# Performance work log

Measured on AMD Instinct MI355X. Metric: run time of the kernel, lower is better.

The kernel has to match this reference:

```python
import jax, jax.numpy as jnp
import numpy as np

B, T, H, NSPK = 8, 1024, 1024, 2
LN_EPS = 1e-5


def setup_inputs() -> dict:
    key = jax.random.key(0)
    ks = jax.random.split(key, 12)
    s = 1.0 / np.sqrt(H)
    return {
        "x": jax.random.normal(ks[0], (B, T, H), jnp.float32),
        "qmask": jax.random.uniform(ks[1], (B, T, NSPK), jnp.float32),
        "dia_len": jax.random.randint(ks[2], (B,), T // 2, T + 1),
        "wp": 8,
        "wf": 8,
        "W_msg": jax.random.normal(ks[3], (H, H), jnp.float32) * s,
        "b_msg": jax.random.normal(ks[4], (H,), jnp.float32) * s,
        "W_self": jax.random.normal(ks[5], (H, H), jnp.float32) * s,
        "b_self": jax.random.normal(ks[6], (H,), jnp.float32) * s,
        "W_out": jax.random.normal(ks[7], (H, H), jnp.float32) * s,
        "b_out": jax.random.normal(ks[8], (H,), jnp.float32) * s,
        "gamma": jnp.ones((H,), jnp.float32),
        "beta": jnp.zeros((H,), jnp.float32),
    }


def reference(x, qmask, dia_len, wp, wf, W_msg, b_msg, W_self, b_self, W_out, b_out, gamma, beta):
    Bb, Tt, Hh = x.shape
    spk = jnp.argmax(qmask, axis=-1)                     # [B,T]
    pos = jnp.arange(Tt)
    offs = jnp.arange(-wp, wf + 1)                       # [W]
    idx = pos[:, None] + offs[None, :]                   # [T,W] window indices
    vlen = dia_len[:, None, None]                        # [B,1,1]
    valid = (idx[None] >= 0) & (idx[None] <= vlen - 1)   # [B,T,W]
    idxc = jnp.clip(idx, 0, Tt - 1)
    nb = jnp.take(x, idxc, axis=1)                       # [B,T,W,H]
    nb_spk = jnp.take(spk, idxc, axis=1)                 # [B,T,W]
    same = (nb_spk == spk[:, :, None]).astype(x.dtype)
    w = jnp.where(valid, 0.5 + 0.5 * same, 0.0)          # speaker weights, masked
    cnt = jnp.maximum(valid.sum(-1).astype(x.dtype), 1.0)  # window sizes [B,T]
    msg = jnp.einsum('btw,btwh->bth', w, nb) / cnt[..., None]
    h = x @ W_self + b_self + msg @ W_msg + b_msg        # per-node fusion
    node_valid = (pos[None, :] < dia_len[:, None])[..., None]
    out = jnp.where(node_valid, h, x)                    # nodes past dia_len keep x
    y = jax.nn.relu(out) @ W_out + b_out                 # dropout = identity (eval)
    z = x + y
    mean = z.mean(-1, keepdims=True)
    var = z.var(-1, keepdims=True)
    return gamma * (z - mean) / jnp.sqrt(var + LN_EPS) + beta
```

## Files before the change

### kernel.cpp

```cpp
#include <hip/hip_runtime.h>


typedef unsigned short u16;
typedef float floatx4 __attribute__((ext_vector_type(4)));
typedef short shortx8 __attribute__((ext_vector_type(8)));

#define T_ 1024
#define H_ 1024

__device__ __forceinline__ float bf2f(u16 v) {
    return __uint_as_float(((unsigned)v) << 16);
}
__device__ __forceinline__ u16 f2bf(float f) {
    unsigned u = __float_as_uint(f);
    return (u16)((u + 0x7fffu + ((u >> 16) & 1u)) >> 16);
}
__device__ __forceinline__ void async16(const void* g, void* l) {
    __builtin_amdgcn_global_load_lds(
        (__attribute__((address_space(1))) void*)g,
        (__attribute__((address_space(3))) void*)l, 16, 0, 0);
}
__device__ __forceinline__ void barrier_mem() {
    asm volatile("" ::: "memory");
    __builtin_amdgcn_s_barrier();
    asm volatile("" ::: "memory");
}

__global__ __launch_bounds__(256)
void transpose_pack(const float* __restrict__ Wself, const float* __restrict__ Wmsg,
                    const float* __restrict__ Wout,
                    u16* __restrict__ wt_cat, u16* __restrict__ wt_out)
{
    __shared__ float s[32][33];
    const int wid = blockIdx.z;
    const float* src = (wid == 0) ? Wself : ((wid == 1) ? Wmsg : Wout);
    const int n0 = blockIdx.x * 32, k0 = blockIdx.y * 32;
    const int tx = threadIdx.x & 31, ty = threadIdx.x >> 5;
#pragma unroll
    for (int i = 0; i < 4; ++i) {
        int k = k0 + ty + 8 * i;
        s[ty + 8 * i][tx] = src[(size_t)k * H_ + n0 + tx];
    }
    __syncthreads();
#pragma unroll
    for (int i = 0; i < 4; ++i) {
        int n = n0 + ty + 8 * i;
        u16 v = f2bf(s[tx][ty + 8 * i]);
        if (wid < 2) wt_cat[(size_t)n * 2048 + wid * 1024 + k0 + tx] = v;
        else         wt_out[(size_t)n * 1024 + k0 + tx] = v;
    }
}

__global__ __launch_bounds__(256)
void msg_pack(const float* __restrict__ x, const float* __restrict__ qmask,
              const int* __restrict__ dia_len, u16* __restrict__ xcat)
{
    __shared__ u16 sx[32][1024];
    const int tid = threadIdx.x;
    const int b = blockIdx.y;
    const int t0 = blockIdx.x * 16;
    const int dlen = dia_len[b];
    const int c4 = tid * 4;
    const float* xb = x + (size_t)b * T_ * H_;

    unsigned spkmask = 0;
#pragma unroll 4
    for (int r = 0; r < 32; ++r) {
        int row = t0 - 8 + r;
        row = row < 0 ? 0 : (row > T_ - 1 ? T_ - 1 : row);
        const float* q = qmask + ((size_t)b * T_ + row) * 2;
        spkmask |= (q[1] > q[0] ? 1u : 0u) << r;
        float4 v = *(const float4*)(xb + (size_t)row * H_ + c4);
        ushort4 u;
        u.x = f2bf(v.x); u.y = f2bf(v.y); u.z = f2bf(v.z); u.w = f2bf(v.w);
        *(ushort4*)&sx[r][c4] = u;
    }
    __syncthreads();

    for (int lt = 0; lt < 16; ++lt) {
        const int t = t0 + lt;
        const unsigned cs = (spkmask >> (lt + 8)) & 1u;
        float a0 = 0.f, a1 = 0.f, a2 = 0.f, a3 = 0.f;
        int cnt = 0;
#pragma unroll
        for (int o = 0; o < 17; ++o) {
            const int idx = t + o - 8;
            if (idx >= 0 && idx < dlen) {
                const float w = (((spkmask >> (lt + o)) & 1u) == cs) ? 1.0f : 0.5f;
                ++cnt;
                ushort4 u = *(const ushort4*)&sx[lt + o][c4];
                a0 += w * bf2f(u.x); a1 += w * bf2f(u.y);
                a2 += w * bf2f(u.z); a3 += w * bf2f(u.w);
            }
        }
        const float inv = 1.0f / (float)(cnt > 0 ? cnt : 1);
        ushort4 m;
        m.x = f2bf(a0 * inv); m.y = f2bf(a1 * inv);
        m.z = f2bf(a2 * inv); m.w = f2bf(a3 * inv);
        const size_t rowg = (size_t)b * T_ + t;
        *(ushort4*)&xcat[rowg * 2048 + 1024 + c4] = m;
        *(ushort4*)&xcat[rowg * 2048 + c4] = *(const ushort4*)&sx[lt + 8][c4];
    }
}

template <int K, int EPI>
__global__ __launch_bounds__(512)
void gemm_bt(const u16* __restrict__ A, const u16* __restrict__ Bt,
             const float* __restrict__ bias1, const float* __restrict__ bias2,
             const float* __restrict__ X, const int* __restrict__ dia_len,
             u16* __restrict__ Rout, float* __restrict__ Zout)
{
    constexpr int NT = K / 64;
    static_assert(NT >= 3, "need >=3 K-tiles for depth-2 prefetch");
    __shared__ u16 sA[3][256 * 64];
    __shared__ u16 sB[3][128 * 64];
    const int tid = threadIdx.x;

    const int bid = blockIdx.x;
    const int li = bid >> 3;
    const int mt = (bid & 7) * 4 + (li >> 3);
    const int nt = li & 7;
    const int bm = mt * 256, bn = nt * 128;

    const int wave = tid >> 6, lane = tid & 63;
    const int wr = wave >> 1, wc = wave & 1;
    const int lrow = lane & 15, lq = lane >> 4;

    const int srow = tid >> 3;
    const int sl   = (tid & 7) ^ (srow & 7);
    const u16* Asrc = A + (size_t)(bm + srow) * K + sl * 8;
    const u16* Bsrc = Bt + (size_t)(bn + srow) * K + sl * 8;

    auto stageA = [&](int t, int buf, int q) {
        async16(Asrc + (size_t)q * 64 * K + t * 64,
                &sA[buf][q * 4096 + tid * 8]);
    };
    auto stageB = [&](int t, int buf, int h) {
        async16(Bsrc + (size_t)h * 64 * K + t * 64,
                &sB[buf][h * 4096 + tid * 8]);
    };

    floatx4 acc[4][4];
#pragma unroll
    for (int i = 0; i < 4; ++i)
#pragma unroll
        for (int j = 0; j < 4; ++j)
            acc[i][j] = (floatx4){0.f, 0.f, 0.f, 0.f};

    const int xk = lrow & 7;
    const int paBase = (wr * 64 + lrow) * 64;
    const int pbBase = (wc * 64 + lrow) * 64;
    const int s0 = ((lq) ^ xk) * 8;
    const int s1 = ((4 + lq) ^ xk) * 8;

    auto tile_body = [&](int t, int cur, int stg, bool do_stage) {
        const u16* curA = &sA[cur][0];
        const u16* curB = &sB[cur][0];
        shortx8 a0[4], b0[4], a1[4], b1[4];
#pragma unroll
        for (int j = 0; j < 4; ++j)
            b0[j] = *(const shortx8*)(curB + pbBase + j * 1024 + s0);
#pragma unroll
        for (int i = 0; i < 4; ++i)
            a0[i] = *(const shortx8*)(curA + paBase + i * 1024 + s0);
        if (do_stage) {
            stageA(t + 2, stg, 0); stageA(t + 2, stg, 1);
            stageA(t + 2, stg, 2); stageA(t + 2, stg, 3);
            stageB(t + 2, stg, 0); stageB(t + 2, stg, 1);
        }
#pragma unroll
        for (int j = 0; j < 4; ++j)
            b1[j] = *(const shortx8*)(curB + pbBase + j * 1024 + s1);
#pragma unroll
        for (int i = 0; i < 4; ++i)
            a1[i] = *(const shortx8*)(curA + paBase + i * 1024 + s1);
        __builtin_amdgcn_s_setprio(1);
#pragma unroll
        for (int i = 0; i < 4; ++i)
#pragma unroll
            for (int j = 0; j < 4; ++j)
                acc[i][j] = __builtin_amdgcn_mfma_f32_16x16x32_bf16(
                    a0[i], b0[j], acc[i][j], 0, 0, 0);
#pragma unroll
        for (int i = 0; i < 4; ++i)
#pragma unroll
            for (int j = 0; j < 4; ++j)
                acc[i][j] = __builtin_amdgcn_mfma_f32_16x16x32_bf16(
                    a1[i], b1[j], acc[i][j], 0, 0, 0);
        __builtin_amdgcn_s_setprio(0);
    };

#pragma unroll
    for (int q = 0; q < 4; ++q) stageA(0, 0, q);
    stageB(0, 0, 0); stageB(0, 0, 1);
#pragma unroll
    for (int q = 0; q < 4; ++q) stageA(1, 1, q);
    stageB(1, 1, 0); stageB(1, 1, 1);
    asm volatile("s_waitcnt vmcnt(6)" ::: "memory");
    barrier_mem();

    int cur = 0, stg = 2;
    for (int t = 0; t < NT - 2; ++t) {
        tile_body(t, cur, stg, true);
        asm volatile("s_waitcnt vmcnt(6)" ::: "memory");
        barrier_mem();
        cur = (cur == 2) ? 0 : cur + 1;
        stg = (stg == 2) ? 0 : stg + 1;
    }
    tile_body(NT - 2, cur, stg, false);
    asm volatile("s_waitcnt vmcnt(0)" ::: "memory");
    barrier_mem();
    cur = (cur == 2) ? 0 : cur + 1;
    tile_body(NT - 1, cur, stg, false);

    const int dl = (EPI == 1) ? dia_len[bm >> 10] : 0;
#pragma unroll
    for (int i = 0; i < 4; ++i) {
        const int row0 = bm + wr * 64 + i * 16 + lq * 4;
#pragma unroll
        for (int j = 0; j < 4; ++j) {
            const int col = bn + wc * 64 + j * 16 + lrow;
#pragma unroll
            for (int r = 0; r < 4; ++r) {
                const int row = row0 + r;
                const float v = acc[i][j][r];
                if (EPI == 1) {
                    const float h = v + bias1[col] + bias2[col];
                    float outv;
                    if ((row & (T_ - 1)) < dl) {
                        outv = h;
                    } else {
                        outv = X[(size_t)row * H_ + col];
                    }
                    Rout[(size_t)row * H_ + col] = f2bf(fmaxf(outv, 0.f));
                } else {
                    const float z = X[(size_t)row * H_ + col] + v + bias1[col];
                    Zout[(size_t)row * H_ + col] = z;
                }
            }
        }
    }
}

__global__ __launch_bounds__(256)
void ln_kernel(const float* __restrict__ Z, const float* __restrict__ gamma,
               const float* __restrict__ beta, float* __restrict__ out)
{
    const int row = blockIdx.x;
    const int tid = threadIdx.x;
    const size_t base = (size_t)row * H_ + tid * 4;
    float4 v = *(const float4*)(Z + base);
    float s = v.x + v.y + v.z + v.w;
    float q = v.x * v.x + v.y * v.y + v.z * v.z + v.w * v.w;
#pragma unroll
    for (int off = 32; off > 0; off >>= 1) {
        s += __shfl_down(s, off);
        q += __shfl_down(q, off);
    }
    __shared__ float ps[4], pq[4];
    const int wave = tid >> 6, lane = tid & 63;
    if (lane == 0) { ps[wave] = s; pq[wave] = q; }
    __syncthreads();
    const float S = ps[0] + ps[1] + ps[2] + ps[3];
    const float Q = pq[0] + pq[1] + pq[2] + pq[3];
    const float mean = S * (1.0f / 1024.0f);
    const float var = Q * (1.0f / 1024.0f) - mean * mean;
    const float inv = rsqrtf(var + 1e-5f);
    float4 g = *(const float4*)(gamma + tid * 4);
    float4 bt = *(const float4*)(beta + tid * 4);
    float4 o;
    o.x = g.x * (v.x - mean) * inv + bt.x;
    o.y = g.y * (v.y - mean) * inv + bt.y;
    o.z = g.z * (v.z - mean) * inv + bt.z;
    o.w = g.w * (v.w - mean) * inv + bt.w;
    *(float4*)(out + base) = o;
}

extern "C" void kernel_launch(void* const* d_in, const int* in_sizes, int n_in,
                              void* d_out, int out_size, void* d_ws, size_t ws_size,
                              hipStream_t stream)
{
    (void)in_sizes; (void)n_in; (void)out_size; (void)ws_size;
    const float* x       = (const float*)d_in[0];
    const float* qmask   = (const float*)d_in[1];
    const int*   dia_len = (const int*)d_in[2];
    const float* W_msg   = (const float*)d_in[5];
    const float* b_msg   = (const float*)d_in[6];
    const float* W_self  = (const float*)d_in[7];
    const float* b_self  = (const float*)d_in[8];
    const float* W_out   = (const float*)d_in[9];
    const float* b_out   = (const float*)d_in[10];
    const float* gamma   = (const float*)d_in[11];
    const float* beta    = (const float*)d_in[12];
    float* out = (float*)d_out;

    char* ws = (char*)d_ws;
    u16*   xcat   = (u16*)ws;
    u16*   rbuf   = (u16*)(ws + (size_t)(32u << 20));
    u16*   wt_cat = (u16*)(ws + (size_t)(48u << 20));
    u16*   wt_out = (u16*)(ws + (size_t)(52u << 20));
    float* zbuf   = (float*)ws;

    transpose_pack<<<dim3(32, 32, 3), 256, 0, stream>>>(W_self, W_msg, W_out, wt_cat, wt_out);
    msg_pack<<<dim3(64, 8), 256, 0, stream>>>(x, qmask, dia_len, xcat);
    gemm_bt<2048, 1><<<dim3(256), 512, 0, stream>>>(xcat, wt_cat, b_self, b_msg,
                                                    x, dia_len, rbuf, nullptr);
    gemm_bt<1024, 2><<<dim3(256), 512, 0, stream>>>(rbuf, wt_out, b_out, nullptr,
                                                    x, nullptr, nullptr, zbuf);
    ln_kernel<<<dim3(8192), 256, 0, stream>>>(zbuf, gamma, beta, out);
}
```

Before: 230.8 us.

## Shrink GEMM tiles to 128x128 with 256 threads and double-buffered LDS

Both GEMMs switch from 256x128 tiles with 512 threads and triple-buffered LDS to 128x128 tiles with 256 threads and double buffering, with 2 blocks per CU and twice as many blocks launched. The K loop now prefetches one tile ahead and drains all loads each iteration. The aim is to cut LDS use and raise occupancy so two blocks can hide each other's latency. The cost is less reuse per tile, more global and L2 traffic, and a shallower prefetch pipeline.

```diff
diff --git a/kernel.cpp b/kernel.cpp
--- a/kernel.cpp
+++ b/kernel.cpp
@@ -104,23 +104,23 @@
 }
 
 template <int K, int EPI>
-__global__ __launch_bounds__(512)
+__global__ __launch_bounds__(256, 2)
 void gemm_bt(const u16* __restrict__ A, const u16* __restrict__ Bt,
              const float* __restrict__ bias1, const float* __restrict__ bias2,
              const float* __restrict__ X, const int* __restrict__ dia_len,
              u16* __restrict__ Rout, float* __restrict__ Zout)
 {
     constexpr int NT = K / 64;
-    static_assert(NT >= 3, "need >=3 K-tiles for depth-2 prefetch");
-    __shared__ u16 sA[3][256 * 64];
-    __shared__ u16 sB[3][128 * 64];
+    static_assert(NT >= 2, "need >=2 K-tiles");
+    __shared__ u16 sA[2][128 * 64];
+    __shared__ u16 sB[2][128 * 64];
     const int tid = threadIdx.x;
 
     const int bid = blockIdx.x;
-    const int li = bid >> 3;
-    const int mt = (bid & 7) * 4 + (li >> 3);
+    const int xcd = bid & 7, li = bid >> 3;
+    const int mt = xcd * 8 + (li >> 3);
     const int nt = li & 7;
-    const int bm = mt * 256, bn = nt * 128;
+    const int bm = mt * 128, bn = nt * 128;
 
     const int wave = tid >> 6, lane = tid & 63;
     const int wr = wave >> 1, wc = wave & 1;
@@ -131,13 +131,14 @@
     const u16* Asrc = A + (size_t)(bm + srow) * K + sl * 8;
     const u16* Bsrc = Bt + (size_t)(bn + srow) * K + sl * 8;
 
-    auto stageA = [&](int t, int buf, int q) {
-        async16(Asrc + (size_t)q * 64 * K + t * 64,
-                &sA[buf][q * 4096 + tid * 8]);
-    };
-    auto stageB = [&](int t, int buf, int h) {
-        async16(Bsrc + (size_t)h * 64 * K + t * 64,
-                &sB[buf][h * 4096 + tid * 8]);
+    auto stage = [&](int t, int buf) {
+        const int k0 = t * 64;
+#pragma unroll
+        for (int q = 0; q < 4; ++q)
+            async16(Asrc + (size_t)q * 32 * K + k0, &sA[buf][q * 2048 + tid * 8]);
+#pragma unroll
+        for (int q = 0; q < 4; ++q)
+            async16(Bsrc + (size_t)q * 32 * K + k0, &sB[buf][q * 2048 + tid * 8]);
     };
 
     floatx4 acc[4][4];
@@ -150,12 +151,19 @@
     const int xk = lrow & 7;
     const int paBase = (wr * 64 + lrow) * 64;
     const int pbBase = (wc * 64 + lrow) * 64;
-    const int s0 = ((lq) ^ xk) * 8;
+    const int s0 = (lq ^ xk) * 8;
     const int s1 = ((4 + lq) ^ xk) * 8;
 
-    auto tile_body = [&](int t, int cur, int stg, bool do_stage) {
-        const u16* curA = &sA[cur][0];
-        const u16* curB = &sB[cur][0];
+    stage(0, 0);
+    stage(1, 1);
+    asm volatile("s_waitcnt vmcnt(8)" ::: "memory");
+    barrier_mem();
+
+    for (int t = 0; t < NT; ++t) {
+        if (t >= 1 && t + 1 < NT) stage(t + 1, (t + 1) & 1);
+
+        const u16* curA = &sA[t & 1][0];
+        const u16* curB = &sB[t & 1][0];
         shortx8 a0[4], b0[4], a1[4], b1[4];
 #pragma unroll
         for (int j = 0; j < 4; ++j)
@@ -163,17 +171,13 @@
 #pragma unroll
         for (int i = 0; i < 4; ++i)
             a0[i] = *(const shortx8*)(curA + paBase + i * 1024 + s0);
-        if (do_stage) {
-            stageA(t + 2, stg, 0); stageA(t + 2, stg, 1);
-            stageA(t + 2, stg, 2); stageA(t + 2, stg, 3);
-            stageB(t + 2, stg, 0); stageB(t + 2, stg, 1);
-        }
 #pragma unroll
         for (int j = 0; j < 4; ++j)
             b1[j] = *(const shortx8*)(curB + pbBase + j * 1024 + s1);
 #pragma unroll
         for (int i = 0; i < 4; ++i)
             a1[i] = *(const shortx8*)(curA + paBase + i * 1024 + s1);
+
         __builtin_amdgcn_s_setprio(1);
 #pragma unroll
         for (int i = 0; i < 4; ++i)
@@ -188,30 +192,12 @@
                 acc[i][j] = __builtin_amdgcn_mfma_f32_16x16x32_bf16(
                     a1[i], b1[j], acc[i][j], 0, 0, 0);
         __builtin_amdgcn_s_setprio(0);
-    };
-
-#pragma unroll
-    for (int q = 0; q < 4; ++q) stageA(0, 0, q);
-    stageB(0, 0, 0); stageB(0, 0, 1);
-#pragma unroll
-    for (int q = 0; q < 4; ++q) stageA(1, 1, q);
-    stageB(1, 1, 0); stageB(1, 1, 1);
-    asm volatile("s_waitcnt vmcnt(6)" ::: "memory");
-    barrier_mem();
-
-    int cur = 0, stg = 2;
-    for (int t = 0; t < NT - 2; ++t) {
-        tile_body(t, cur, stg, true);
-        asm volatile("s_waitcnt vmcnt(6)" ::: "memory");
-        barrier_mem();
-        cur = (cur == 2) ? 0 : cur + 1;
-        stg = (stg == 2) ? 0 : stg + 1;
-    }
-    tile_body(NT - 2, cur, stg, false);
-    asm volatile("s_waitcnt vmcnt(0)" ::: "memory");
-    barrier_mem();
-    cur = (cur == 2) ? 0 : cur + 1;
-    tile_body(NT - 1, cur, stg, false);
+
+        if (t + 1 < NT) {
+            asm volatile("s_waitcnt vmcnt(0)" ::: "memory");
+            barrier_mem();
+        }
+    }
 
     const int dl = (EPI == 1) ? dia_len[bm >> 10] : 0;
 #pragma unroll
@@ -303,9 +289,9 @@
 
     transpose_pack<<<dim3(32, 32, 3), 256, 0, stream>>>(W_self, W_msg, W_out, wt_cat, wt_out);
     msg_pack<<<dim3(64, 8), 256, 0, stream>>>(x, qmask, dia_len, xcat);
-    gemm_bt<2048, 1><<<dim3(256), 512, 0, stream>>>(xcat, wt_cat, b_self, b_msg,
+    gemm_bt<2048, 1><<<dim3(512), 256, 0, stream>>>(xcat, wt_cat, b_self, b_msg,
                                                     x, dia_len, rbuf, nullptr);
-    gemm_bt<1024, 2><<<dim3(256), 512, 0, stream>>>(rbuf, wt_out, b_out, nullptr,
+    gemm_bt<1024, 2><<<dim3(512), 256, 0, stream>>>(rbuf, wt_out, b_out, nullptr,
                                                     x, nullptr, nullptr, zbuf);
     ln_kernel<<<dim3(8192), 256, 0, stream>>>(zbuf, gamma, beta, out);
 }
```

Measured after the change: 223.1 us. -3.3%, faster.
